# Optimization experiments

Measured on AMD Instinct MI355X. Metric: run time of the kernel, lower is better.

## Reference

```python
import jax, jax.numpy as jnp
import numpy as np
from itertools import permutations, combinations

BATCH = 32768
EPS = 1e-06  # positivity eps from __init__


def _levi_civita7():
    e = np.zeros((7,) * 7, dtype=np.float32)
    for p in permutations(range(7)):
        inv = sum(1 for i in range(7) for j in range(i + 1, 7) if p[i] > p[j])
        e[p] = -1.0 if inv % 2 else 1.0
    return jnp.asarray(e)

_EPS7 = _levi_civita7()  # (7,7,7,7,7,7,7) rank-7 Levi-Civita tensor
_TRIPLES = np.array(list(combinations(range(7), 3)), dtype=np.int32)  # (35,3) i<j<k index triples
_PERMS3 = [((0, 1, 2), 1.0), ((1, 2, 0), 1.0), ((2, 0, 1), 1.0),
           ((0, 2, 1), -1.0), ((2, 1, 0), -1.0), ((1, 0, 2), -1.0)]


def _phi_full(phi):
    # expand 35 independent components to fully antisymmetric (B,7,7,7)
    b = phi.shape[0]
    pf = jnp.zeros((b, 7, 7, 7), phi.dtype)
    for perm, s in _PERMS3:
        ia = _TRIPLES[:, perm[0]]
        ib = _TRIPLES[:, perm[1]]
        ic = _TRIPLES[:, perm[2]]
        pf = pf.at[:, ia, ib, ic].set(s * phi)
    return pf


def _metric_from_phi(phi):
    # Standard G2 metric: B_ij = (1/144) phi_ikl phi_jmn phi_pqr eps^{klmnpqr};
    # g = B / |det B|^{1/9}  (unit-determinant normalization)
    pf = _phi_full(phi)  # (B,7,7,7)
    C = jnp.einsum('klmnpqr,bpqr->bklmn', _EPS7, pf)  # (B,7,7,7,7)
    T = jnp.einsum('bklmn,bjmn->bklj', C, pf)          # (B,7,7,7)
    Bm = jnp.einsum('bikl,bklj->bij', pf, T) / 144.0   # (B,7,7)
    det = jnp.linalg.det(Bm)
    g = Bm / (jnp.abs(det)[:, None, None] + 1e-12) ** (1.0 / 9.0)
    return 0.5 * (g + jnp.swapaxes(g, -1, -2))  # exact symmetry for eigvalsh


def setup_inputs() -> dict:
    key = jax.random.key(0)
    phi = jax.random.normal(key, (BATCH, 35), dtype=jnp.float32)
    return {"phi": phi}


def reference(phi):
    g = _metric_from_phi(phi)              # (B,7,7)
    ev = jnp.linalg.eigvalsh(g)            # (B,7)
    return jax.nn.relu(-ev + EPS).sum(axis=-1)  # (B,) sum of negative-eigenvalue violations
```

## Files before the change

### kernel.cpp

```cpp
#include <hip/hip_runtime.h>
#include <utility>

#define BATCH 32768
#define NPHI 35
#define SWEEPS 6

constexpr int choose2(int n){ return (n*(n-1))/2; }

constexpr int tri_id_sorted(int a,int b,int c){
  int id=0;
  for(int x=0;x<a;++x) id += choose2(6-x);
  for(int y=a+1;y<b;++y) id += (6-y);
  id += (c-b-1);
  return id;
}

constexpr int tri_id3(int a,int b,int c){
  int x=a,y=b,z=c;
  if (x>y){int t=x;x=y;y=t;}
  if (y>z){int t=y;y=z;z=t;}
  if (x>y){int t=x;x=y;y=t;}
  return tri_id_sorted(x,y,z);
}

constexpr int sgn3(int a,int b,int c){
  int inv = (a>b)+(a>c)+(b>c);
  return (inv&1)? -1 : 1;
}

constexpr int UT(int i,int j){
  return i*7 - (i*(i-1))/2 + (j-i);
}

constexpr int pair_k(int g){
  int idx=0;
  for(int k=0;k<7;++k) for(int l=k+1;l<7;++l){ if(idx==g) return k; ++idx; }
  return 0;
}
constexpr int pair_l(int g){
  int idx=0;
  for(int k=0;k<7;++k) for(int l=k+1;l<7;++l){ if(idx==g) return l; ++idx; }
  return 0;
}

struct GProg {
  int nt, nb;
  signed char t_dst[50], t_a[50], t_b[50], t_s[50]; unsigned char t_init[50];
  signed char b_dst[26], b_a[26], b_b[26], b_s[26];
};

constexpr GProg build_group(int k,int l){
  GProg P{}; P.nt=0; P.nb=0;
  bool tinit[7]={};
  for(int m=0;m<7;++m) for(int n2=m+1;n2<7;++n2){
    if(m==k||m==l||n2==k||n2==l) continue;
    int comp[3]={0,0,0}; int cn=0;
    for(int x=0;x<7;++x) if(x!=k&&x!=l&&x!=m&&x!=n2){ comp[cn]=x; ++cn; }
    int perm[7]={k,l,m,n2,comp[0],comp[1],comp[2]};
    int invc=0;
    for(int i=0;i<7;++i) for(int j=i+1;j<7;++j) if(perm[i]>perm[j]) ++invc;
    const int es=(invc&1)? -1 : 1;
    const int tcomp=tri_id_sorted(comp[0],comp[1],comp[2]);
    for(int j=0;j<7;++j){
      if(j==m||j==n2) continue;
      P.t_dst[P.nt]=(signed char)j;
      P.t_a [P.nt]=(signed char)tcomp;
      P.t_b [P.nt]=(signed char)tri_id3(j,m,n2);
      P.t_s [P.nt]=(signed char)(es*sgn3(j,m,n2));
      P.t_init[P.nt]=tinit[j]?0:1; tinit[j]=true;
      ++P.nt;
    }
  }
  for(int i=0;i<7;++i){
    if(i==k||i==l) continue;
    for(int j=i;j<7;++j){
      P.b_dst[P.nb]=(signed char)UT(i,j);
      P.b_a [P.nb]=(signed char)tri_id3(i,k,l);
      P.b_b [P.nb]=(signed char)j;
      P.b_s [P.nb]=(signed char)sgn3(i,k,l);
      ++P.nb;
    }
  }
  return P;
}

template<int G> inline constexpr GProg GP = build_group(pair_k(G), pair_l(G));

template<int G,int Q>
__device__ __forceinline__ void t_step(float (&T)[7], const float (&ph)[NPHI]){
  constexpr int d=GP<G>.t_dst[Q], a=GP<G>.t_a[Q], b=GP<G>.t_b[Q];
  constexpr bool neg=(GP<G>.t_s[Q]<0), ini=(GP<G>.t_init[Q]!=0);
  const float x = neg ? -ph[a] : ph[a];
  if constexpr (ini) T[d] = x*ph[b];
  else               T[d] = fmaf(x, ph[b], T[d]);
}

template<int G,int Q>
__device__ __forceinline__ void b_step(float (&U)[28], const float (&T)[7],
                                       const float (&ph)[NPHI]){
  constexpr int d=GP<G>.b_dst[Q], a=GP<G>.b_a[Q], b=GP<G>.b_b[Q];
  constexpr bool neg=(GP<G>.b_s[Q]<0);
  const float x = neg ? -ph[a] : ph[a];
  U[d] = fmaf(x, T[b], U[d]);
}

template<int G,int... TQ>
__device__ __forceinline__ void run_t(float (&T)[7], const float (&ph)[NPHI],
                                      std::integer_sequence<int,TQ...>){
  (t_step<G,TQ>(T,ph), ...);
}
template<int G,int... BQ>
__device__ __forceinline__ void run_b(float (&U)[28], const float (&T)[7],
                                      const float (&ph)[NPHI],
                                      std::integer_sequence<int,BQ...>){
  (b_step<G,BQ>(U,T,ph), ...);
}

template<int G>
__device__ __forceinline__ void do_group(float (&U)[28], const float (&ph)[NPHI]){
  float T[7];
  run_t<G>(T, ph, std::make_integer_sequence<int, GP<G>.nt>{});
  run_b<G>(U, T, ph, std::make_integer_sequence<int, GP<G>.nb>{});
  __builtin_amdgcn_sched_barrier(0);
}

template<int... G>
__device__ __forceinline__ void all_groups(float (&U)[28], const float (&ph)[NPHI],
                                           std::integer_sequence<int,G...>){
  (do_group<G>(U,ph), ...);
}

template<int R>
__device__ __forceinline__ void jrot_t(float (&A)[28]){
  constexpr int p1 = pair_k(R), q1 = pair_l(R);
  const float apq = A[UT(p1,q1)];
  const float app = A[UT(p1,p1)];
  const float aqq = A[UT(q1,q1)];
  const float s2  = apq + apq;
  const float h   = aqq - app;
  const float r   = __builtin_amdgcn_sqrtf(fmaf(s2, s2, h*h));
  const float den = h + __builtin_copysignf(r + 1e-38f, h);
  const float t   = s2 * __builtin_amdgcn_rcpf(den);
  const float c   = __builtin_amdgcn_rsqf(fmaf(t, t, 1.0f));
  const float s   = t*c;
  A[UT(p1,p1)] = fmaf(-t, apq, app);
  A[UT(q1,q1)] = fmaf( t, apq, aqq);
  A[UT(p1,q1)] = 0.0f;
  #pragma unroll
  for (int r2=0;r2<7;++r2){
    if (r2==p1 || r2==q1) continue;
    const int irp = (r2<p1)? UT(r2,p1) : UT(p1,r2);
    const int irq = (r2<q1)? UT(r2,q1) : UT(q1,r2);
    const float arp = A[irp], arq = A[irq];
    A[irp] = fmaf(c, arp, -(s*arq));
    A[irq] = fmaf(c, arq,  (s*arp));
  }
}

template<int... R>
__device__ __forceinline__ void jacobi_sweep(float (&A)[28],
                                             std::integer_sequence<int,R...>){
  (jrot_t<R>(A), ...);
}

__device__ __forceinline__ float finish(const float (&A)[28]){
  float det = 1.0f;
  #pragma unroll
  for (int i=0;i<7;++i) det *= A[UT(i,i)];
  const float ad = fabsf(det) + 1e-12f;
  const float scale = __builtin_amdgcn_exp2f(__builtin_amdgcn_logf(ad) * (1.0f/9.0f));
  const float inv = __builtin_amdgcn_rcpf(scale);
  float sum = 0.0f;
  #pragma unroll
  for (int i=0;i<7;++i){
    const float ev = A[UT(i,i)]*inv;
    sum += fmaxf(1e-6f - ev, 0.0f);
  }
  return sum;
}

__global__ __launch_bounds__(64,1)
void PositivityConstraint_89086211654295_kernel(const float* __restrict__ phi,
                                                float* __restrict__ out){
  const int lane = threadIdx.x;
  const int gid  = blockIdx.x*64 + lane;

  __shared__ float lph[64*36];
  const float* __restrict__ gbase = phi + (size_t)blockIdx.x * 64 * NPHI;
  #pragma unroll
  for (int i=0;i<NPHI;++i){
    const int idx = i*64 + lane;
    lph[(idx/NPHI)*36 + (idx%NPHI)] = gbase[idx];
  }
  __syncthreads();

  float ph[NPHI];
  #pragma unroll
  for (int i=0;i<NPHI;++i) ph[i] = lph[lane*36 + i];

  float U[28];
  #pragma unroll
  for (int i=0;i<28;++i) U[i]=0.f;

  all_groups(U, ph, std::make_integer_sequence<int,21>{});

  float A[28];
  #pragma unroll
  for (int i=0;i<28;++i) A[i] = U[i]*(1.0f/6.0f);

  for (int sweep=0; sweep<SWEEPS; ++sweep){
    jacobi_sweep(A, std::make_integer_sequence<int,21>{});
  }

  out[gid] = finish(A);
}

extern "C" void kernel_launch(void* const* d_in, const int* in_sizes, int n_in,
                              void* d_out, int out_size, void* d_ws, size_t ws_size,
                              hipStream_t stream) {
  const float* phi = (const float*)d_in[0];
  float* out = (float*)d_out;
  (void)in_sizes; (void)n_in; (void)out_size; (void)d_ws; (void)ws_size;
  hipLaunchKernelGGL(PositivityConstraint_89086211654295_kernel,
                     dim3(BATCH/64), dim3(64), 0, stream, phi, out);
}
```

Before: 67.35 us.

## Use round-robin parallel Jacobi ordering with independent rotation angles per round

Replaces the cyclic row-by-row Jacobi sweep with a round-robin (chess tournament) ordering. Each sweep is 7 rounds of 3 disjoint pivot pairs, and all three rotation angles in a round are computed before any rotation is applied. This exposes instruction-level parallelism: the sqrt, rcp and rsq dependency chains of three rotations can overlap instead of running strictly one after another. The trade-off is that the parallel ordering may converge differently per sweep while keeping the same six-sweep count, which could affect accuracy.

```diff
diff --git a/kernel.cpp b/kernel.cpp
--- a/kernel.cpp
+++ b/kernel.cpp
@@ -42,6 +42,9 @@
   for(int k=0;k<7;++k) for(int l=k+1;l<7;++l){ if(idx==g) return l; ++idx; }
   return 0;
 }
+
+constexpr int rr_p(int r,int s){ int a=(r+1+s)%7, b=(r+6-s)%7; return a<b?a:b; }
+constexpr int rr_q(int r,int s){ int a=(r+1+s)%7, b=(r+6-s)%7; return a<b?b:a; }
 
 struct GProg {
   int nt, nb;
@@ -130,37 +133,56 @@
   (do_group<G>(U,ph), ...);
 }
 
-template<int R>
-__device__ __forceinline__ void jrot_t(float (&A)[28]){
-  constexpr int p1 = pair_k(R), q1 = pair_l(R);
-  const float apq = A[UT(p1,q1)];
-  const float app = A[UT(p1,p1)];
-  const float aqq = A[UT(q1,q1)];
+template<int P,int Q>
+__device__ __forceinline__ void jangle(const float (&A)[28],
+                                       float &t, float &c, float &s){
+  const float apq = A[UT(P,Q)];
+  const float app = A[UT(P,P)];
+  const float aqq = A[UT(Q,Q)];
   const float s2  = apq + apq;
   const float h   = aqq - app;
   const float r   = __builtin_amdgcn_sqrtf(fmaf(s2, s2, h*h));
   const float den = h + __builtin_copysignf(r + 1e-38f, h);
-  const float t   = s2 * __builtin_amdgcn_rcpf(den);
-  const float c   = __builtin_amdgcn_rsqf(fmaf(t, t, 1.0f));
-  const float s   = t*c;
-  A[UT(p1,p1)] = fmaf(-t, apq, app);
-  A[UT(q1,q1)] = fmaf( t, apq, aqq);
-  A[UT(p1,q1)] = 0.0f;
+  t = s2 * __builtin_amdgcn_rcpf(den);
+  c = __builtin_amdgcn_rsqf(fmaf(t, t, 1.0f));
+  s = t*c;
+}
+
+template<int P,int Q>
+__device__ __forceinline__ void japply(float (&A)[28], float t, float c, float s){
+  const float apq = A[UT(P,Q)];
+  A[UT(P,P)] = fmaf(-t, apq, A[UT(P,P)]);
+  A[UT(Q,Q)] = fmaf( t, apq, A[UT(Q,Q)]);
+  A[UT(P,Q)] = 0.0f;
   #pragma unroll
   for (int r2=0;r2<7;++r2){
-    if (r2==p1 || r2==q1) continue;
-    const int irp = (r2<p1)? UT(r2,p1) : UT(p1,r2);
-    const int irq = (r2<q1)? UT(r2,q1) : UT(q1,r2);
+    if (r2==P || r2==Q) continue;
+    const int irp = (r2<P)? UT(r2,P) : UT(P,r2);
+    const int irq = (r2<Q)? UT(r2,Q) : UT(Q,r2);
     const float arp = A[irp], arq = A[irq];
     A[irp] = fmaf(c, arp, -(s*arq));
     A[irq] = fmaf(c, arq,  (s*arp));
   }
 }
 
+template<int R>
+__device__ __forceinline__ void jround(float (&A)[28]){
+  constexpr int p0=rr_p(R,0), q0=rr_q(R,0);
+  constexpr int p1=rr_p(R,1), q1=rr_q(R,1);
+  constexpr int p2=rr_p(R,2), q2=rr_q(R,2);
+  float t0,c0,s0, t1,c1,s1, t2,c2,s2;
+  jangle<p0,q0>(A, t0,c0,s0);
+  jangle<p1,q1>(A, t1,c1,s1);
+  jangle<p2,q2>(A, t2,c2,s2);
+  japply<p0,q0>(A, t0,c0,s0);
+  japply<p1,q1>(A, t1,c1,s1);
+  japply<p2,q2>(A, t2,c2,s2);
+}
+
 template<int... R>
-__device__ __forceinline__ void jacobi_sweep(float (&A)[28],
-                                             std::integer_sequence<int,R...>){
-  (jrot_t<R>(A), ...);
+__device__ __forceinline__ void jsweep(float (&A)[28],
+                                       std::integer_sequence<int,R...>){
+  (jround<R>(A), ...);
 }
 
 __device__ __forceinline__ float finish(const float (&A)[28]){
@@ -209,7 +231,7 @@
   for (int i=0;i<28;++i) A[i] = U[i]*(1.0f/6.0f);
 
   for (int sweep=0; sweep<SWEEPS; ++sweep){
-    jacobi_sweep(A, std::make_integer_sequence<int,21>{});
+    jsweep(A, std::make_integer_sequence<int,7>{});
   }
 
   out[gid] = finish(A);
```

Result: no change. 66.23 us (-1.7%).
